# Kernel optimization log

Measured on AMD Instinct MI355X. Metric: run time of the kernel, lower is better.

Reference implementation:

```python
import jax, jax.numpy as jnp
import numpy as np

D_MODEL = 2048
N_HEADS = 16
HEAD_DIM = D_MODEL // N_HEADS
ROPE_BASE = 10000.0


def rope(x):
    # x: [b, h, s, d]; matches the torch module exactly:
    # x1 = even dims, x2 = odd dims; output = concat([x1*cos - x2*sin, x1*sin + x2*cos], -1)
    b, h, s, d = x.shape
    theta = 1.0 / ROPE_BASE ** (jnp.arange(0, d, 2, dtype=jnp.float32) / d)  # [d/2]
    angles = jnp.arange(s, dtype=jnp.float32)[:, None] * theta[None, :]       # [s, d/2]
    cos = jnp.cos(angles)[None, None]  # [1,1,s,d/2]
    sin = jnp.sin(angles)[None, None]
    x1, x2 = x[..., ::2], x[..., 1::2]
    return jnp.concatenate([x1 * cos - x2 * sin, x1 * sin + x2 * cos], axis=-1)


def setup_inputs() -> dict:
    key = jax.random.key(0)
    ks = jax.random.split(key, 5)
    b, s = 2, 2048
    x = jax.random.normal(ks[0], (b, s, D_MODEL), dtype=jnp.float32)
    scale_in = 1.0 / np.sqrt(D_MODEL)
    Wqkv = jax.random.normal(ks[1], (D_MODEL, 3 * D_MODEL), dtype=jnp.float32) * scale_in
    bqkv = jnp.zeros((3 * D_MODEL,), dtype=jnp.float32)
    Wo = jax.random.normal(ks[2], (D_MODEL, D_MODEL), dtype=jnp.float32) * scale_in
    bo = jnp.zeros((D_MODEL,), dtype=jnp.float32)
    return {"x": x, "Wqkv": Wqkv, "bqkv": bqkv, "Wo": Wo, "bo": bo}


def reference(x, Wqkv, bqkv, Wo, bo):
    b, s, d = x.shape
    qkv = x @ Wqkv + bqkv                      # [b, s, 3d]
    q, k, v = jnp.split(qkv, 3, axis=-1)
    def to_heads(t):
        return t.reshape(b, s, N_HEADS, HEAD_DIM).transpose(0, 2, 1, 3)  # [b,h,s,hd]
    q, k, v = to_heads(q), to_heads(k), to_heads(v)
    q = rope(q)
    k = rope(k)
    scores = jnp.einsum('bhqd,bhkd->bhqk', q, k) / jnp.sqrt(jnp.float32(HEAD_DIM))
    attn = jax.nn.softmax(scores, axis=-1)
    out = jnp.einsum('bhqk,bhkd->bhqd', attn, v)
    out = out.transpose(0, 2, 1, 3).reshape(b, s, d)
    return out @ Wo + bo
```

## Files before the change

kernel.cpp:

```cpp
#include <hip/hip_runtime.h>
#include <hip/hip_bf16.h>
#include <cstdint>
#include <type_traits>

#define D_MODEL 2048
#define NH 16
#define HD 128
#define SEQ 2048
#define QKV_LD (3 * D_MODEL)

typedef __attribute__((ext_vector_type(8))) short short8;
typedef __attribute__((ext_vector_type(4))) float f32x4;
typedef __attribute__((ext_vector_type(16))) float f32x16;

__device__ __forceinline__ ushort f2bf(float f) {
    union { float f; uint32_t u; } c; c.f = f;
    uint32_t u = c.u;
    uint32_t r = (u + 0x7FFFu + ((u >> 16) & 1u)) >> 16;
    return (ushort)r;
}
__device__ __forceinline__ float bf2f(ushort b) {
    union { uint32_t u; float f; } c; c.u = ((uint32_t)b) << 16;
    return c.f;
}

__device__ __forceinline__ void load_lds16(const ushort* g, ushort* l) {
    __builtin_amdgcn_global_load_lds(
        (const __attribute__((address_space(1))) void*)g,
        (__attribute__((address_space(3))) void*)l, 16, 0, 0);
}

__global__ void cvt_bf16_kernel(const float* __restrict__ in, ushort* __restrict__ out, int n4) {
    int idx = blockIdx.x * blockDim.x + threadIdx.x;
    if (idx >= n4) return;
    float4 v = ((const float4*)in)[idx];
    ushort4 o;
    o.x = f2bf(v.x); o.y = f2bf(v.y); o.z = f2bf(v.z); o.w = f2bf(v.w);
    ((ushort4*)out)[idx] = o;
}

__global__ void transpose_bf16_kernel(const float* __restrict__ in, ushort* __restrict__ out,
                                      int R, int C) {
    __shared__ float tile[32][33];
    int tx = threadIdx.x, ty = threadIdx.y;
    int c0 = blockIdx.x * 32, r0 = blockIdx.y * 32;
    for (int i = 0; i < 4; ++i) {
        int r = r0 + ty + i * 8;
        tile[ty + i * 8][tx] = in[(size_t)r * C + c0 + tx];
    }
    __syncthreads();
    for (int i = 0; i < 4; ++i) {
        int c = c0 + ty + i * 8;
        out[(size_t)c * R + r0 + tx] = f2bf(tile[tx][ty + i * 8]);
    }
}

#define WAITV(N) asm volatile("s_waitcnt vmcnt(" #N ")" ::: "memory")
#define BARF()   do { __builtin_amdgcn_s_barrier(); \
                      asm volatile("" ::: "memory"); } while (0)
#define PRIO1    __builtin_amdgcn_s_setprio(1)
#define PRIO0    __builtin_amdgcn_s_setprio(0)

#define B_ROWOFF(L) (NHALF == 2 ? (((L) & 1) * 128 + ((L) >> 1) * 32) : ((L) * 64))
#define STAGE_A(L, T_, B_) load_lds16(Ag + (size_t)(L) * 64 * K + (size_t)(T_) * 64, \
                                      smA + (B_) * 16384 + (L) * 4096 + ldsW)
#define STAGE_B(L, T_, B_) load_lds16(Bg + (size_t)B_ROWOFF(L) * K + (size_t)(T_) * 64, \
                                      smB + (B_) * (8192 * NHALF) + (L) * 4096 + ldsW)
#define READ_A(MH) do { const ushort* _ab = smA + cb * 16384 + aRow + (MH) * 4096; \
    _Pragma("unroll") for (int i_ = 0; i_ < 4; ++i_) { \
        af[i_][0] = *(const short8*)(_ab + i_ * 1024 + pc0); \
        af[i_][1] = *(const short8*)(_ab + i_ * 1024 + pc1); } } while (0)
#define READ_BH(dst, NHh) do { const ushort* _bb = smB + cb * (8192 * NHALF) + (NHh) * 8192 + bRow; \
    _Pragma("unroll") for (int j_ = 0; j_ < 2; ++j_) { \
        dst[j_][0] = *(const short8*)(_bb + j_ * 1024 + pc0); \
        dst[j_][1] = *(const short8*)(_bb + j_ * 1024 + pc1); } } while (0)
#define MFMA_PH(MH, NHh, bf) do { \
    _Pragma("unroll") for (int i_ = 0; i_ < 4; ++i_) \
    _Pragma("unroll") for (int j_ = 0; j_ < 2; ++j_) { \
        acc[(MH) * 4 + i_][(NHh) * 2 + j_] = __builtin_amdgcn_mfma_f32_16x16x32_bf16( \
            af[i_][0], bf[j_][0], acc[(MH) * 4 + i_][(NHh) * 2 + j_], 0, 0, 0); \
        acc[(MH) * 4 + i_][(NHh) * 2 + j_] = __builtin_amdgcn_mfma_f32_16x16x32_bf16( \
            af[i_][1], bf[j_][1], acc[(MH) * 4 + i_][(NHh) * 2 + j_], 0, 0, 0); } } while (0)

template <typename OutT, int NHALF>
__global__ __launch_bounds__(512, 2) void gemm256(
    const ushort* __restrict__ A,
    const ushort* __restrict__ Bt,
    const float* __restrict__ bias,
    OutT* __restrict__ C,
    int M, int N, int K)
{
    __shared__ __align__(16) ushort sm[32768 + 2 * 8192 * NHALF];
    ushort* smA = sm;
    ushort* smB = sm + 32768;

    int t = threadIdx.x;
    int w = t >> 6, lane = t & 63;
    int lr = lane & 15, lh = lane >> 4;
    int wm_idx = w >> 2, wn_idx = w & 3;
    int m0 = blockIdx.y * 256, n0 = blockIdx.x * (128 * NHALF);

    int srow = t >> 3;
    int scol = ((t & 7) ^ (srow & 7)) << 3;
    const ushort* Ag = A + (size_t)(m0 + srow) * K + scol;
    int bq = (NHALF == 2) ? ((srow >> 5) * 64 + (srow & 31)) : srow;
    const ushort* Bg = Bt + (size_t)(n0 + bq) * K + scol;
    int ldsW = w * 512;

    int pc0 = (lh ^ (lr & 7)) << 3;
    int pc1 = ((4 + lh) ^ (lr & 7)) << 3;
    int aRow = (wm_idx * 128 + lr) * 64;
    int bRow = (wn_idx * 32 + lr) * 64;

    f32x4 acc[8][2 * NHALF];
#pragma unroll
    for (int i = 0; i < 8; ++i)
#pragma unroll
        for (int j = 0; j < 2 * NHALF; ++j) acc[i][j] = (f32x4)0.0f;
    short8 af[4][2], bf0[2][2], bf1[2][2];

    int NT = K >> 6;

    if constexpr (NHALF == 2) {
        STAGE_A(0, 0, 0); STAGE_A(2, 0, 0); STAGE_B(0, 0, 0); STAGE_B(1, 0, 0);
        STAGE_B(2, 0, 0); STAGE_B(3, 0, 0);
        STAGE_A(1, 0, 0); STAGE_A(3, 0, 0);
        WAITV(4);
    } else {
        STAGE_A(0, 0, 0); STAGE_A(2, 0, 0); STAGE_B(0, 0, 0);
        STAGE_B(1, 0, 0); STAGE_A(1, 0, 0); STAGE_A(3, 0, 0);
        WAITV(2);
    }
    BARF();

    for (int T = 0; T < NT; ++T) {
        int cb = T & 1, nb = cb ^ 1;
        bool pf = (T + 1 < NT);
        if constexpr (NHALF == 2) {
            READ_A(0); READ_BH(bf0, 0);
            if (pf) { STAGE_A(0, T + 1, nb); STAGE_A(2, T + 1, nb);
                      STAGE_B(0, T + 1, nb); STAGE_B(1, T + 1, nb); }
            BARF();
            PRIO1; MFMA_PH(0, 0, bf0); PRIO0;
            if (pf) WAITV(6); else WAITV(2);
            BARF();
            READ_BH(bf1, 1);
            if (pf) { STAGE_B(2, T + 1, nb); STAGE_B(3, T + 1, nb); }
            BARF();
            PRIO1; MFMA_PH(0, 1, bf1); PRIO0;
            if (pf) WAITV(6); else WAITV(0);
            BARF();
            READ_A(1);
            if (pf) { STAGE_A(1, T + 1, nb); STAGE_A(3, T + 1, nb); }
            BARF();
            PRIO1; MFMA_PH(1, 1, bf1); MFMA_PH(1, 0, bf0); PRIO0;
            if (pf) WAITV(4);
            BARF();
        } else {
            READ_A(0); READ_BH(bf0, 0);
            if (pf) { STAGE_A(0, T + 1, nb); STAGE_A(2, T + 1, nb); STAGE_B(0, T + 1, nb); }
            BARF();
            PRIO1; MFMA_PH(0, 0, bf0); PRIO0;
            if (pf) WAITV(3); else WAITV(0);
            BARF();
            READ_A(1);
            if (pf) { STAGE_B(1, T + 1, nb); STAGE_A(1, T + 1, nb); STAGE_A(3, T + 1, nb); }
            BARF();
            PRIO1; MFMA_PH(1, 0, bf0); PRIO0;
            if (pf) WAITV(2);
            BARF();
        }
    }

    float bv[2 * NHALF];
#pragma unroll
    for (int jj = 0; jj < 2 * NHALF; ++jj) bv[jj] = bias[n0 + wn_idx * 32 * NHALF + jj * 16 + lr];
#pragma unroll
    for (int ii = 0; ii < 8; ++ii) {
        int row = m0 + wm_idx * 128 + ii * 16 + lh * 4;
#pragma unroll
        for (int jj = 0; jj < 2 * NHALF; ++jj) {
            int col = n0 + wn_idx * 32 * NHALF + jj * 16 + lr;
#pragma unroll
            for (int r = 0; r < 4; ++r) {
                float v = acc[ii][jj][r] + bv[jj];
                if constexpr (std::is_same<OutT, ushort>::value)
                    C[(size_t)(row + r) * N + col] = f2bf(v);
                else
                    C[(size_t)(row + r) * N + col] = v;
            }
        }
    }
}

__global__ void rope_table(float2* __restrict__ tab) {
    int i = blockIdx.x * blockDim.x + threadIdx.x;
    int s = i >> 6, j = i & 63;
    float theta = powf(10000.0f, -(float)j * (1.0f / 64.0f));
    float ang = (float)s * theta;
    float sn, cs;
    sincosf(ang, &sn, &cs);
    tab[i] = make_float2(cs, sn);
}

__global__ void rope_cast_qk(const ushort* __restrict__ qkv,
                             const float2* __restrict__ tab,
                             ushort* __restrict__ Qb, ushort* __restrict__ Kb) {
    int t = threadIdx.x;
    int wv = blockIdx.x * 4 + (t >> 6);
    int j = t & 63;
    int bs = wv >> 5;
    int rem = wv & 31;
    int which = rem >> 4;
    int h = rem & 15;
    int s = bs & 2047;
    int b = bs >> 11;
    size_t src = (size_t)bs * QKV_LD + which * D_MODEL + h * HD;
    uint32_t pr = *(const uint32_t*)(qkv + src + 2 * j);
    float x1 = bf2f((ushort)(pr & 0xffff));
    float x2 = bf2f((ushort)(pr >> 16));
    float2 cspair = tab[(s << 6) + j];
    float cs = cspair.x, sn = cspair.y;
    float sc = which ? 1.0f : 0.08838834764831845f;
    float o1 = (x1 * cs - x2 * sn) * sc;
    float o2 = (x1 * sn + x2 * cs) * sc;
    ushort* dst = which ? Kb : Qb;
    size_t obase = ((size_t)(b * NH + h) * SEQ + s) * HD;
    dst[obase + j] = f2bf(o1);
    dst[obase + 64 + j] = f2bf(o2);
}

__global__ void v_transpose(const ushort* __restrict__ qkv, ushort* __restrict__ Vt) {
    __shared__ ushort tile[32][33];
    int tx = threadIdx.x, ty = threadIdx.y;
    int s0 = blockIdx.x * 32;
    int d0 = blockIdx.y * 32;
    int bh = blockIdx.z;
    int b = bh >> 4, h = bh & 15;
    for (int i = 0; i < 4; ++i) {
        int s = s0 + ty + i * 8;
        tile[ty + i * 8][tx] = qkv[((size_t)(b * SEQ + s)) * QKV_LD + 2 * D_MODEL + h * HD + d0 + tx];
    }
    __syncthreads();
    for (int i = 0; i < 4; ++i) {
        int d = d0 + ty + i * 8;
        Vt[((size_t)bh * HD + d) * SEQ + s0 + tx] = tile[tx][ty + i * 8];
    }
}

__global__ __launch_bounds__(256) void attn_mfma(const ushort* __restrict__ Qb,
                                                 const ushort* __restrict__ Kb,
                                                 const ushort* __restrict__ Vt,
                                                 ushort* __restrict__ ctx) {
    __shared__ ushort smem[25600];
    ushort* Ks = smem;
    ushort* Vts = smem + 8192;
    ushort* Ps = smem + 16384;

    int t = threadIdx.x;
    int w = t >> 6, l = t & 63;
    int l31 = l & 31, g = l >> 5;
    int q0 = blockIdx.x * 128;
    int bh = blockIdx.y;
    int b = bh >> 4, h = bh & 15;

    int qrow = q0 + w * 32 + l31;
    const ushort* Qg = Qb + ((size_t)bh * SEQ + qrow) * HD;
    short8 qf[8];
#pragma unroll
    for (int kc = 0; kc < 8; kc++)
        qf[kc] = *(const short8*)(Qg + kc * 16 + g * 8);

    f32x16 O[4];
#pragma unroll
    for (int di = 0; di < 4; di++) O[di] = (f32x16)0.0f;
    float m_run = -INFINITY, l_run = 0.0f;

    const ushort* KgB = Kb + (size_t)bh * SEQ * HD;
    const ushort* VtB = Vt + (size_t)bh * HD * SEQ;

    for (int k0 = 0; k0 < SEQ; k0 += 64) {
        __syncthreads();
#pragma unroll
        for (int c2 = 0; c2 < 4; c2++) {
            int f = c2 * 256 + t;
            int r = f >> 4, c = f & 15;
            int cp = c ^ (r & 15);
            uint4 v = *(const uint4*)(KgB + (size_t)(k0 + r) * HD + c * 8);
            *(uint4*)(Ks + r * 128 + cp * 8) = v;
        }
#pragma unroll
        for (int c2 = 0; c2 < 4; c2++) {
            int f = c2 * 256 + t;
            int d = f >> 3, c = f & 7;
            int cp = c ^ (d & 7);
            uint4 v = *(const uint4*)(VtB + (size_t)d * SEQ + k0 + c * 8);
            *(uint4*)(Vts + d * 64 + cp * 8) = v;
        }
        __syncthreads();

        f32x16 St[2];
        St[0] = (f32x16)0.0f;
        St[1] = (f32x16)0.0f;
#pragma unroll
        for (int ki = 0; ki < 2; ki++) {
            int row = ki * 32 + l31;
#pragma unroll
            for (int kc = 0; kc < 8; kc++) {
                int cp = (kc * 2 + g) ^ (row & 15);
                short8 a = *(const short8*)(Ks + row * 128 + cp * 8);
                St[ki] = __builtin_amdgcn_mfma_f32_32x32x16_bf16(a, qf[kc], St[ki], 0, 0, 0);
            }
        }

        float mx = -INFINITY;
#pragma unroll
        for (int ki = 0; ki < 2; ki++)
#pragma unroll
            for (int r = 0; r < 16; r++) mx = fmaxf(mx, St[ki][r]);
        mx = fmaxf(mx, __shfl_xor(mx, 32));
        float mn = fmaxf(m_run, mx);
        float alpha = __expf(m_run - mn);
        m_run = mn;
        float psum = 0.0f;
#pragma unroll
        for (int ki = 0; ki < 2; ki++)
#pragma unroll
            for (int r = 0; r < 16; r++) {
                float p = __expf(St[ki][r] - mn);
                St[ki][r] = p;
                psum += p;
            }
        psum += __shfl_xor(psum, 32);
        l_run = l_run * alpha + psum;
#pragma unroll
        for (int di = 0; di < 4; di++)
#pragma unroll
            for (int r = 0; r < 16; r++) O[di][r] *= alpha;

        {
            int qloc = w * 32 + l31;
            ushort* Pr = Ps + qloc * 72;
#pragma unroll
            for (int ki = 0; ki < 2; ki++)
#pragma unroll
                for (int u = 0; u < 4; u++) {
                    ushort4 pk;
                    pk.x = f2bf(St[ki][4 * u + 0]);
                    pk.y = f2bf(St[ki][4 * u + 1]);
                    pk.z = f2bf(St[ki][4 * u + 2]);
                    pk.w = f2bf(St[ki][4 * u + 3]);
                    *(ushort4*)(Pr + ki * 32 + 8 * u + 4 * g) = pk;
                }
        }

        {
            int qloc = w * 32 + l31;
            short8 pb[4];
#pragma unroll
            for (int kc = 0; kc < 4; kc++)
                pb[kc] = *(const short8*)(Ps + qloc * 72 + kc * 16 + g * 8);
#pragma unroll
            for (int di = 0; di < 4; di++) {
                int d = di * 32 + l31;
#pragma unroll
                for (int kc = 0; kc < 4; kc++) {
                    int cp = (kc * 2 + g) ^ (d & 7);
                    short8 va = *(const short8*)(Vts + d * 64 + cp * 8);
                    O[di] = __builtin_amdgcn_mfma_f32_32x32x16_bf16(va, pb[kc], O[di], 0, 0, 0);
                }
            }
        }
    }

    __syncthreads();
    float inv = 1.0f / l_run;
    ushort* ob = smem;
    {
        int qloc = w * 32 + l31;
        ushort* orow = ob + qloc * 128;
#pragma unroll
        for (int di = 0; di < 4; di++)
#pragma unroll
            for (int u = 0; u < 4; u++) {
                ushort4 pk;
                pk.x = f2bf(O[di][4 * u + 0] * inv);
                pk.y = f2bf(O[di][4 * u + 1] * inv);
                pk.z = f2bf(O[di][4 * u + 2] * inv);
                pk.w = f2bf(O[di][4 * u + 3] * inv);
                *(ushort4*)(orow + di * 32 + 8 * u + 4 * g) = pk;
            }
    }
#pragma unroll
    for (int p = 0; p < 8; p++) {
        int qloc = w * 32 + p * 4 + (l >> 4);
        int c16 = l & 15;
        uint4 v = *(const uint4*)(ob + qloc * 128 + c16 * 8);
        size_t tok = (size_t)b * SEQ + q0 + qloc;
        *(uint4*)(ctx + tok * D_MODEL + h * HD + c16 * 8) = v;
    }
}

extern "C" void kernel_launch(void* const* d_in, const int* in_sizes, int n_in,
                              void* d_out, int out_size, void* d_ws, size_t ws_size,
                              hipStream_t stream) {
    const float* x    = (const float*)d_in[0];
    const float* Wqkv = (const float*)d_in[1];
    const float* bqkv = (const float*)d_in[2];
    const float* Wo   = (const float*)d_in[3];
    const float* bo   = (const float*)d_in[4];
    float* out = (float*)d_out;

    char* ws = (char*)d_ws;
    ushort* x_bf   = (ushort*)(ws);
    ushort* wqkvT  = (ushort*)(ws + 16777216);
    ushort* woT    = (ushort*)(ws + 41943040);
    ushort* qkv_bf = (ushort*)(ws + 50331648);
    ushort* Qb     = (ushort*)(ws + 100663296);
    ushort* Kb     = (ushort*)(ws + 117440512);
    ushort* VtG    = (ushort*)(ws + 134217728);
    ushort* ctx    = (ushort*)(ws + 150994944);
    float2* rtab   = (float2*)(ws + 150994944);

    rope_table<<<512, 256, 0, stream>>>(rtab);
    cvt_bf16_kernel<<<8192, 256, 0, stream>>>(x, x_bf, 2097152);
    transpose_bf16_kernel<<<dim3(192, 64), dim3(32, 8), 0, stream>>>(Wqkv, wqkvT, 2048, 6144);
    transpose_bf16_kernel<<<dim3(64, 64), dim3(32, 8), 0, stream>>>(Wo, woT, 2048, 2048);
    gemm256<ushort, 2><<<dim3(24, 16), 512, 0, stream>>>(x_bf, wqkvT, bqkv, qkv_bf, 4096, 6144, 2048);
    rope_cast_qk<<<32768, 256, 0, stream>>>(qkv_bf, rtab, Qb, Kb);
    v_transpose<<<dim3(64, 4, 32), dim3(32, 8), 0, stream>>>(qkv_bf, VtG);
    attn_mfma<<<dim3(16, 32), 256, 0, stream>>>(Qb, Kb, VtG, ctx);
    gemm256<float, 1><<<dim3(16, 16), 512, 0, stream>>>(ctx, woT, bo, out, 4096, 2048, 2048);
}
```

Before: 430.6 us.

## Add 128x384-tile QKV GEMM with 2 blocks/CU and MFMA priority in attention

Adds a new gemm384 kernel for the QKV projection using 128x384 output tiles, a double-buffered LDS pipeline staged in three phases, and launch bounds allowing two blocks per CU. It replaces the 256x256-tile gemm256 launch, giving 512 blocks instead of 384 so that work is spread more evenly across the 256 CUs. Separately, it raises wave priority around the MFMA loops in the attention kernel. Smaller tiles lower arithmetic intensity per block, and the hand-tuned vmcnt waits must match the exact load counts to stay correct.

```diff
diff --git a/kernel.cpp b/kernel.cpp
--- a/kernel.cpp
+++ b/kernel.cpp
@@ -29,6 +29,12 @@
         (const __attribute__((address_space(1))) void*)g,
         (__attribute__((address_space(3))) void*)l, 16, 0, 0);
 }
+
+#define WAITV(N) asm volatile("s_waitcnt vmcnt(" #N ")" ::: "memory")
+#define BARF()   do { __builtin_amdgcn_s_barrier(); \
+                      asm volatile("" ::: "memory"); } while (0)
+#define PRIO1    __builtin_amdgcn_s_setprio(1)
+#define PRIO0    __builtin_amdgcn_s_setprio(0)
 
 __global__ void cvt_bf16_kernel(const float* __restrict__ in, ushort* __restrict__ out, int n4) {
     int idx = blockIdx.x * blockDim.x + threadIdx.x;
@@ -54,12 +60,6 @@
         out[(size_t)c * R + r0 + tx] = f2bf(tile[tx][ty + i * 8]);
     }
 }
-
-#define WAITV(N) asm volatile("s_waitcnt vmcnt(" #N ")" ::: "memory")
-#define BARF()   do { __builtin_amdgcn_s_barrier(); \
-                      asm volatile("" ::: "memory"); } while (0)
-#define PRIO1    __builtin_amdgcn_s_setprio(1)
-#define PRIO0    __builtin_amdgcn_s_setprio(0)
 
 #define B_ROWOFF(L) (NHALF == 2 ? (((L) & 1) * 128 + ((L) >> 1) * 32) : ((L) * 64))
 #define STAGE_A(L, T_, B_) load_lds16(Ag + (size_t)(L) * 64 * K + (size_t)(T_) * 64, \
@@ -188,6 +188,111 @@
                     C[(size_t)(row + r) * N + col] = f2bf(v);
                 else
                     C[(size_t)(row + r) * N + col] = v;
+            }
+        }
+    }
+}
+
+#define STAGE_A3(L, T_, B_) load_lds16(Ag + (size_t)(L) * 64 * K + (size_t)(T_) * 64, \
+                                       smA + (B_) * 8192 + (L) * 4096 + ldsW)
+#define STAGE_B3(L, T_, B_) load_lds16(Bg + (size_t)((((L) & 1) * 2 + wnp) * 96 + ((L) >> 1) * 32 + rb) * K + (size_t)(T_) * 64, \
+                                       smB + (B_) * 24576 + (L) * 4096 + ldsW)
+#define READ_A3() do { const ushort* _ab = smA + cb * 8192 + aRow; \
+    _Pragma("unroll") for (int i_ = 0; i_ < 4; ++i_) { \
+        af[i_][0] = *(const short8*)(_ab + i_ * 1024 + pc0); \
+        af[i_][1] = *(const short8*)(_ab + i_ * 1024 + pc1); } } while (0)
+#define READ_B3(H) do { const ushort* _bb = smB + cb * 24576 + (H) * 8192 + bRow; \
+    _Pragma("unroll") for (int j_ = 0; j_ < 2; ++j_) { \
+        bfr[j_][0] = *(const short8*)(_bb + j_ * 1024 + pc0); \
+        bfr[j_][1] = *(const short8*)(_bb + j_ * 1024 + pc1); } } while (0)
+#define MFMA_P3(H) do { \
+    _Pragma("unroll") for (int i_ = 0; i_ < 4; ++i_) \
+    _Pragma("unroll") for (int j_ = 0; j_ < 2; ++j_) { \
+        acc[i_][(H) * 2 + j_] = __builtin_amdgcn_mfma_f32_16x16x32_bf16( \
+            af[i_][0], bfr[j_][0], acc[i_][(H) * 2 + j_], 0, 0, 0); \
+        acc[i_][(H) * 2 + j_] = __builtin_amdgcn_mfma_f32_16x16x32_bf16( \
+            af[i_][1], bfr[j_][1], acc[i_][(H) * 2 + j_], 0, 0, 0); } } while (0)
+
+__global__ __launch_bounds__(512, 2) void gemm384(
+    const ushort* __restrict__ A,
+    const ushort* __restrict__ Bt,
+    const float* __restrict__ bias,
+    ushort* __restrict__ C,
+    int M, int N, int K)
+{
+    __shared__ __align__(16) ushort sm[65536];
+    ushort* smA = sm;
+    ushort* smB = sm + 16384;
+
+    int t = threadIdx.x;
+    int w = t >> 6, lane = t & 63;
+    int lr = lane & 15, lh = lane >> 4;
+    int wm_idx = w >> 2, wn_idx = w & 3;
+    int m0 = blockIdx.y * 128, n0 = blockIdx.x * 384;
+
+    int srow = t >> 3;
+    int scol = ((t & 7) ^ (srow & 7)) << 3;
+    const ushort* Ag = A + (size_t)(m0 + srow) * K + scol;
+    const ushort* Bg = Bt + (size_t)n0 * K + scol;
+    int wnp = srow >> 5;
+    int rb = srow & 31;
+    int ldsW = w * 512;
+
+    int pc0 = (lh ^ (lr & 7)) << 3;
+    int pc1 = ((4 + lh) ^ (lr & 7)) << 3;
+    int aRow = (wm_idx * 64 + lr) * 64;
+    int bRow = (wn_idx * 32 + lr) * 64;
+
+    f32x4 acc[4][6];
+#pragma unroll
+    for (int i = 0; i < 4; ++i)
+#pragma unroll
+        for (int j = 0; j < 6; ++j) acc[i][j] = (f32x4)0.0f;
+    short8 af[4][2], bfr[2][2];
+
+    int NT = K >> 6;
+
+    STAGE_A3(0, 0, 0); STAGE_A3(1, 0, 0); STAGE_B3(0, 0, 0); STAGE_B3(1, 0, 0);
+    STAGE_B3(2, 0, 0); STAGE_B3(3, 0, 0); STAGE_B3(4, 0, 0); STAGE_B3(5, 0, 0);
+    WAITV(4);
+    BARF();
+
+    for (int T = 0; T < NT; ++T) {
+        int cb = T & 1, nb = cb ^ 1;
+        bool pf = (T + 1 < NT);
+        READ_A3(); READ_B3(0);
+        if (pf) { STAGE_A3(0, T + 1, nb); STAGE_A3(1, T + 1, nb); STAGE_B3(0, T + 1, nb); }
+        BARF();
+        PRIO1; MFMA_P3(0); PRIO0;
+        if (pf) WAITV(5); else WAITV(2);
+        BARF();
+        READ_B3(1);
+        if (pf) { STAGE_B3(1, T + 1, nb); STAGE_B3(2, T + 1, nb); STAGE_B3(3, T + 1, nb); }
+        BARF();
+        PRIO1; MFMA_P3(1); PRIO0;
+        if (pf) WAITV(6); else WAITV(0);
+        BARF();
+        READ_B3(2);
+        if (pf) { STAGE_B3(4, T + 1, nb); STAGE_B3(5, T + 1, nb); }
+        BARF();
+        PRIO1; MFMA_P3(2); PRIO0;
+        if (pf) WAITV(4);
+        BARF();
+    }
+
+    float bv[6];
+#pragma unroll
+    for (int jj = 0; jj < 6; ++jj) bv[jj] = bias[n0 + wn_idx * 96 + jj * 16 + lr];
+#pragma unroll
+    for (int ii = 0; ii < 4; ++ii) {
+        int row = m0 + wm_idx * 64 + ii * 16 + lh * 4;
+#pragma unroll
+        for (int jj = 0; jj < 6; ++jj) {
+            int col = n0 + wn_idx * 96 + jj * 16 + lr;
+#pragma unroll
+            for (int r = 0; r < 4; ++r) {
+                float v = acc[ii][jj][r] + bv[jj];
+                C[(size_t)(row + r) * N + col] = f2bf(v);
             }
         }
     }
@@ -302,6 +407,7 @@
         f32x16 St[2];
         St[0] = (f32x16)0.0f;
         St[1] = (f32x16)0.0f;
+        PRIO1;
 #pragma unroll
         for (int ki = 0; ki < 2; ki++) {
             int row = ki * 32 + l31;
@@ -312,6 +418,7 @@
                 St[ki] = __builtin_amdgcn_mfma_f32_32x32x16_bf16(a, qf[kc], St[ki], 0, 0, 0);
             }
         }
+        PRIO0;
 
         float mx = -INFINITY;
 #pragma unroll
@@ -360,6 +467,7 @@
 #pragma unroll
             for (int kc = 0; kc < 4; kc++)
                 pb[kc] = *(const short8*)(Ps + qloc * 72 + kc * 16 + g * 8);
+            PRIO1;
 #pragma unroll
             for (int di = 0; di < 4; di++) {
                 int d = di * 32 + l31;
@@ -370,6 +478,7 @@
                     O[di] = __builtin_amdgcn_mfma_f32_32x32x16_bf16(va, pb[kc], O[di], 0, 0, 0);
                 }
             }
+            PRIO0;
         }
     }
 
@@ -426,7 +535,7 @@
     cvt_bf16_kernel<<<8192, 256, 0, stream>>>(x, x_bf, 2097152);
     transpose_bf16_kernel<<<dim3(192, 64), dim3(32, 8), 0, stream>>>(Wqkv, wqkvT, 2048, 6144);
     transpose_bf16_kernel<<<dim3(64, 64), dim3(32, 8), 0, stream>>>(Wo, woT, 2048, 2048);
-    gemm256<ushort, 2><<<dim3(24, 16), 512, 0, stream>>>(x_bf, wqkvT, bqkv, qkv_bf, 4096, 6144, 2048);
+    gemm384<<<dim3(16, 32), 512, 0, stream>>>(x_bf, wqkvT, bqkv, qkv_bf, 4096, 6144, 2048);
     rope_cast_qk<<<32768, 256, 0, stream>>>(qkv_bf, rtab, Qb, Kb);
     v_transpose<<<dim3(64, 4, 32), dim3(32, 8), 0, stream>>>(qkv_bf, VtG);
     attn_mfma<<<dim3(16, 32), 256, 0, stream>>>(Qb, Kb, VtG, ctx);
```

New measurement: 423.4 us. Within noise of the previous version (-1.7%).
